# Optimization experiments

Hardware: AMD Instinct MI355X
Metric: run time of the kernel (lower is better)

The kernel has to match this reference:

```python
import jax, jax.numpy as jnp
import numpy as np

C_CURV = 1.0  # hyperbolic curvature (init kwarg c)
EPS = 1e-7


def _to_ball(v, max_norm=0.8):
    # rescale rows to lie strictly inside the unit Poincare ball
    n = jnp.linalg.norm(v, axis=-1, keepdims=True)
    return v * (max_norm / (n + 1.0))


def setup_inputs() -> dict:
    key = jax.random.key(0)
    k1, k2 = jax.random.split(key)
    B, C, D = 32768, 2048, 512
    z_mix = _to_ball(jax.random.normal(k1, (B, D), dtype=jnp.float32))
    prototypes = _to_ball(jax.random.normal(k2, (C, D), dtype=jnp.float32))
    repel_margin = jnp.float32(2.0)
    return {"z_mix": z_mix, "prototypes": prototypes, "repel_margin": repel_margin}


def dist_matrix(x, y, c):
    # Poincare-ball pairwise distance (arccosh form):
    # d(x,y) = arccosh(1 + 2c||x-y||^2 / ((1-c||x||^2)(1-c||y||^2))) / sqrt(c)
    x2 = jnp.sum(x * x, axis=-1)            # (B,)
    y2 = jnp.sum(y * y, axis=-1)            # (C,)
    xy = jnp.einsum('bd,cd->bc', x, y)      # (B, C)
    sqdist = jnp.maximum(x2[:, None] + y2[None, :] - 2.0 * xy, 0.0)
    denom = (1.0 - c * x2)[:, None] * (1.0 - c * y2)[None, :]
    arg = 1.0 + 2.0 * c * sqdist / jnp.maximum(denom, EPS)
    return jnp.arccosh(jnp.maximum(arg, 1.0 + EPS)) / jnp.sqrt(c)


def reference(z_mix, prototypes, repel_margin):
    dist2proto = dist_matrix(z_mix, prototypes, C_CURV)   # (B, C)
    min_dist = jnp.min(dist2proto, axis=1)                # (B,)
    return jnp.mean(jax.nn.relu(repel_margin - min_dist))
```

## Files before the change

kernel.cpp:

```cpp
#include <hip/hip_runtime.h>
#include <stdint.h>

#define EPS_F 1e-7f

typedef float f32x4 __attribute__((ext_vector_type(4)));

union A8 { uint2 u2; long l; };

__device__ __forceinline__ unsigned cvt4(float a, float b, float c, float d) {
  int v = __builtin_amdgcn_cvt_pk_fp8_f32(a, b, 0, false);
  return (unsigned)__builtin_amdgcn_cvt_pk_fp8_f32(c, d, v, true);
}

__global__ __launch_bounds__(256) void prep_kernel(
    const float* __restrict__ protos, uint8_t* __restrict__ wsB,
    float* __restrict__ y2a, float* __restrict__ rya,
    float* __restrict__ out) {
  const int lane = threadIdx.x & 63;
  const int w    = threadIdx.x >> 6;
  const int kp2  = lane >> 2, q = lane & 3;
  const int sl0  = 8 * kp2 + q;
  const int sl1  = sl0 + 4;
#pragma unroll
  for (int i = 0; i < 4; ++i) {
    int c = (blockIdx.x * 4 + w) * 4 + i;
    const float4* p = (const float4*)(protos + (size_t)c * 512 + lane * 8);
    float4 f0 = p[0], f1 = p[1];
    float s = f0.x*f0.x + f0.y*f0.y + f0.z*f0.z + f0.w*f0.w
            + f1.x*f1.x + f1.y*f1.y + f1.z*f1.z + f1.w*f1.w;
#pragma unroll
    for (int off = 32; off > 0; off >>= 1) s += __shfl_xor(s, off, 64);
    if (lane == 0) { y2a[c] = s; rya[c] = 1.f / (1.f - s); }
    unsigned ux = cvt4(f0.x, f0.y, f0.z, f0.w);
    unsigned uy = cvt4(f1.x, f1.y, f1.z, f1.w);
    uint4 ch;
    ch.x = __shfl((int)ux, sl0, 64);
    ch.y = __shfl((int)uy, sl0, 64);
    ch.z = __shfl((int)ux, sl1, 64);
    ch.w = __shfl((int)uy, sl1, 64);
    if (lane < 32) {
      int g = c >> 4, cl = c & 15;
      ((uint4*)wsB)[((size_t)g * 8 + kp2) * 64 + q * 16 + cl] = ch;
    }
  }
  if (blockIdx.x == 0 && threadIdx.x == 0) out[0] = 0.f;
}

__global__ __launch_bounds__(256, 2) void gemm_min_kernel(
    const float* __restrict__ z, const uint8_t* __restrict__ wsB,
    const float* __restrict__ y2a, const float* __restrict__ rya,
    const float* __restrict__ marg, float* __restrict__ out) {
  __shared__ uint8_t As[32 * 1024];
  __shared__ float x2s[64];
  __shared__ float rxs[64];
  __shared__ float minbuf[64][4];

  const int tid  = threadIdx.x;
  const int lane = tid & 63;
  const int w    = tid >> 6;
  const int q    = lane >> 4;
  const int l15  = lane & 15;
  const size_t rowbase = (size_t)blockIdx.x * 64;

  {
    const float* rp0 = z + (rowbase + w * 16 + l15) * 512;
    float s = 0.f;
#pragma unroll
    for (int j = 0; j < 8; ++j) {
      const float* rp = rp0 + j * 64 + q * 8;
      float4 a0 = ((const float4*)rp)[0];
      float4 a1 = ((const float4*)rp)[1];
      float4 b0 = ((const float4*)(rp + 32))[0];
      float4 b1 = ((const float4*)(rp + 32))[1];
      s += a0.x*a0.x + a0.y*a0.y + a0.z*a0.z + a0.w*a0.w
         + a1.x*a1.x + a1.y*a1.y + a1.z*a1.z + a1.w*a1.w
         + b0.x*b0.x + b0.y*b0.y + b0.z*b0.z + b0.w*b0.w
         + b1.x*b1.x + b1.y*b1.y + b1.z*b1.z + b1.w*b1.w;
      uint4 ch;
      ch.x = cvt4(a0.x, a0.y, a0.z, a0.w);
      ch.y = cvt4(a1.x, a1.y, a1.z, a1.w);
      ch.z = cvt4(b0.x, b0.y, b0.z, b0.w);
      ch.w = cvt4(b1.x, b1.y, b1.z, b1.w);
      ((uint4*)As)[(j * 4 + w) * 64 + lane] = ch;
    }
    s += __shfl_xor(s, 16, 64);
    s += __shfl_xor(s, 32, 64);
    if (lane < 16) { x2s[w * 16 + lane] = s; rxs[w * 16 + lane] = 1.f / (1.f - s); }
  }
  __syncthreads();

  float x2r[4][4];
#pragma unroll
  for (int rf = 0; rf < 4; ++rf) {
    float4 x4 = *(const float4*)&x2s[rf * 16 + q * 4];
    x2r[rf][0] = x4.x; x2r[rf][1] = x4.y; x2r[rf][2] = x4.z; x2r[rf][3] = x4.w;
  }

  const uint4* Ap = (const uint4*)As;
  const uint4* Bg = (const uint4*)wsB;

  uint4 B0w[4], B1w[4];
#pragma unroll
  for (int i = 0; i < 4; ++i) {
    B0w[i] = Bg[(size_t)(w * 256 + i) * 64 + lane];
    B1w[i] = Bg[(size_t)(w * 256 + 8 + i) * 64 + lane];
  }

  float tmin[4][4];
#pragma unroll
  for (int rf = 0; rf < 4; ++rf)
#pragma unroll
    for (int r = 0; r < 4; ++r) tmin[rf][r] = 3.4e38f;

  const float* y2p = y2a + w * 512 + l15;
  const float* ryp = rya + w * 512 + l15;

#pragma clang loop unroll(disable)
  for (int s = 0; s < 16; ++s) {
    f32x4 acc[4][2];
#pragma unroll
    for (int rf = 0; rf < 4; ++rf) {
      f32x4 z4 = {0.f, 0.f, 0.f, 0.f};
      acc[rf][0] = z4; acc[rf][1] = z4;
    }
    float y2v0 = y2p[s * 32],      ryv0 = ryp[s * 32];
    float y2v1 = y2p[s * 32 + 16], ryv1 = ryp[s * 32 + 16];

#pragma unroll
    for (int kp2 = 0; kp2 < 8; ++kp2) {
      uint4 bu0 = B0w[kp2 & 3];
      uint4 bu1 = B1w[kp2 & 3];
      {
        int ip = s * 8 + kp2 + 4;
        int sp = ip >> 3, kq = ip & 7;
        size_t c0 = (size_t)(w * 256 + sp * 16 + kq) * 64 + lane;
        B0w[kp2 & 3] = Bg[c0];
        B1w[kp2 & 3] = Bg[c0 + 8 * 64];
      }
      A8 b0lo, b0hi, b1lo, b1hi;
      b0lo.u2 = make_uint2(bu0.x, bu0.y); b0hi.u2 = make_uint2(bu0.z, bu0.w);
      b1lo.u2 = make_uint2(bu1.x, bu1.y); b1hi.u2 = make_uint2(bu1.z, bu1.w);
#pragma unroll
      for (int rf = 0; rf < 4; ++rf) {
        uint4 av = Ap[(kp2 * 4 + rf) * 64 + lane];
        A8 alo, ahi;
        alo.u2 = make_uint2(av.x, av.y);
        ahi.u2 = make_uint2(av.z, av.w);
        acc[rf][0] = __builtin_amdgcn_mfma_f32_16x16x32_fp8_fp8(
            alo.l, b0lo.l, acc[rf][0], 0, 0, 0);
        acc[rf][1] = __builtin_amdgcn_mfma_f32_16x16x32_fp8_fp8(
            alo.l, b1lo.l, acc[rf][1], 0, 0, 0);
        acc[rf][0] = __builtin_amdgcn_mfma_f32_16x16x32_fp8_fp8(
            ahi.l, b0hi.l, acc[rf][0], 0, 0, 0);
        acc[rf][1] = __builtin_amdgcn_mfma_f32_16x16x32_fp8_fp8(
            ahi.l, b1hi.l, acc[rf][1], 0, 0, 0);
      }
    }

#pragma unroll
    for (int rf = 0; rf < 4; ++rf) {
#pragma unroll
      for (int r = 0; r < 4; ++r) {
        float xv = x2r[rf][r];
        float u0 = fmaxf(fmaf(-2.f, acc[rf][0][r], xv + y2v0), 0.f) * ryv0;
        float u1 = fmaxf(fmaf(-2.f, acc[rf][1][r], xv + y2v1), 0.f) * ryv1;
        tmin[rf][r] = fminf(tmin[rf][r], fminf(u0, u1));
      }
    }
  }

#pragma unroll
  for (int rf = 0; rf < 4; ++rf) {
#pragma unroll
    for (int r = 0; r < 4; ++r) {
      float v = tmin[rf][r];
      v = fminf(v, __shfl_xor(v, 1, 64));
      v = fminf(v, __shfl_xor(v, 2, 64));
      v = fminf(v, __shfl_xor(v, 4, 64));
      v = fminf(v, __shfl_xor(v, 8, 64));
      if (l15 == 0) minbuf[rf * 16 + q * 4 + r][w] = v;
    }
  }
  __syncthreads();

  if (w == 0) {
    float m = fminf(fminf(minbuf[lane][0], minbuf[lane][1]),
                    fminf(minbuf[lane][2], minbuf[lane][3]));
    float t = m * rxs[lane];
    float arg = fmaxf(fmaf(2.f, t, 1.f), 1.f + EPS_F);
    float contrib = fmaxf(marg[0] - acoshf(arg), 0.f);
#pragma unroll
    for (int off = 32; off > 0; off >>= 1) contrib += __shfl_xor(contrib, off, 64);
    if (lane == 0) atomicAdd(out, contrib * (1.0f / 32768.f));
  }
}

extern "C" void kernel_launch(void* const* d_in, const int* in_sizes, int n_in,
                              void* d_out, int out_size, void* d_ws, size_t ws_size,
                              hipStream_t stream) {
  const float* z      = (const float*)d_in[0];
  const float* protos = (const float*)d_in[1];
  const float* marg   = (const float*)d_in[2];
  float* out = (float*)d_out;
  uint8_t* wsB = (uint8_t*)d_ws;
  float* y2a = (float*)((char*)d_ws + (1 << 20) + 192 * 1024);
  float* rya = y2a + 2048;

  prep_kernel<<<128, 256, 0, stream>>>(protos, wsB, y2a, rya, out);
  gemm_min_kernel<<<512, 256, 0, stream>>>(z, wsB, y2a, rya, marg, out);
}
```

Baseline: 154.5 us.

## Split prototype dimension across two blocks per row slab with atomicMin merge

Each 64-row slab is now handled by two blocks, one per half of the prototypes, doubling the grid to 1024 blocks. The per-row minimum is merged through an atomicMin on float bits in a workspace, and a new final kernel applies acosh, the margin relu and the mean. Launch bounds are raised to 4 blocks per CU and the x2 values are reloaded from shared memory instead of held in registers, which lowers register pressure. The cost is that each half re-reads and re-converts the z slab to fp8, plus a third kernel launch and extra global atomics.

```diff
diff --git a/kernel.cpp b/kernel.cpp
--- a/kernel.cpp
+++ b/kernel.cpp
@@ -15,7 +15,7 @@
 __global__ __launch_bounds__(256) void prep_kernel(
     const float* __restrict__ protos, uint8_t* __restrict__ wsB,
     float* __restrict__ y2a, float* __restrict__ rya,
-    float* __restrict__ out) {
+    unsigned* __restrict__ minws, float* __restrict__ out) {
   const int lane = threadIdx.x & 63;
   const int w    = threadIdx.x >> 6;
   const int kp2  = lane >> 2, q = lane & 3;
@@ -43,16 +43,16 @@
       ((uint4*)wsB)[((size_t)g * 8 + kp2) * 64 + q * 16 + cl] = ch;
     }
   }
+  minws[blockIdx.x * 256 + threadIdx.x] = 0x7F800000u;
   if (blockIdx.x == 0 && threadIdx.x == 0) out[0] = 0.f;
 }
 
-__global__ __launch_bounds__(256, 2) void gemm_min_kernel(
+__global__ __launch_bounds__(256, 4) void gemm_min_kernel(
     const float* __restrict__ z, const uint8_t* __restrict__ wsB,
     const float* __restrict__ y2a, const float* __restrict__ rya,
-    const float* __restrict__ marg, float* __restrict__ out) {
+    unsigned* __restrict__ minws, float* __restrict__ x2ws) {
   __shared__ uint8_t As[32 * 1024];
   __shared__ float x2s[64];
-  __shared__ float rxs[64];
   __shared__ float minbuf[64][4];
 
   const int tid  = threadIdx.x;
@@ -60,7 +60,9 @@
   const int w    = tid >> 6;
   const int q    = lane >> 4;
   const int l15  = lane & 15;
-  const size_t rowbase = (size_t)blockIdx.x * 64;
+  const int half = blockIdx.x >> 9;
+  const int slab = blockIdx.x & 511;
+  const size_t rowbase = (size_t)slab * 64;
 
   {
     const float* rp0 = z + (rowbase + w * 16 + l15) * 512;
@@ -85,25 +87,21 @@
     }
     s += __shfl_xor(s, 16, 64);
     s += __shfl_xor(s, 32, 64);
-    if (lane < 16) { x2s[w * 16 + lane] = s; rxs[w * 16 + lane] = 1.f / (1.f - s); }
+    if (lane < 16) {
+      x2s[w * 16 + lane] = s;
+      if (half == 0) x2ws[rowbase + w * 16 + lane] = s;
+    }
   }
   __syncthreads();
 
-  float x2r[4][4];
-#pragma unroll
-  for (int rf = 0; rf < 4; ++rf) {
-    float4 x4 = *(const float4*)&x2s[rf * 16 + q * 4];
-    x2r[rf][0] = x4.x; x2r[rf][1] = x4.y; x2r[rf][2] = x4.z; x2r[rf][3] = x4.w;
-  }
-
   const uint4* Ap = (const uint4*)As;
-  const uint4* Bg = (const uint4*)wsB;
+  const uint4* Bgw = (const uint4*)wsB + ((size_t)(half * 512 + w * 128)) * 64 + lane;
 
   uint4 B0w[4], B1w[4];
 #pragma unroll
   for (int i = 0; i < 4; ++i) {
-    B0w[i] = Bg[(size_t)(w * 256 + i) * 64 + lane];
-    B1w[i] = Bg[(size_t)(w * 256 + 8 + i) * 64 + lane];
+    B0w[i] = Bgw[(size_t)i * 64];
+    B1w[i] = Bgw[(size_t)(i + 8) * 64];
   }
 
   float tmin[4][4];
@@ -112,11 +110,11 @@
 #pragma unroll
     for (int r = 0; r < 4; ++r) tmin[rf][r] = 3.4e38f;
 
-  const float* y2p = y2a + w * 512 + l15;
-  const float* ryp = rya + w * 512 + l15;
+  const float* y2p = y2a + half * 1024 + w * 256 + l15;
+  const float* ryp = rya + half * 1024 + w * 256 + l15;
 
 #pragma clang loop unroll(disable)
-  for (int s = 0; s < 16; ++s) {
+  for (int s = 0; s < 8; ++s) {
     f32x4 acc[4][2];
 #pragma unroll
     for (int rf = 0; rf < 4; ++rf) {
@@ -133,9 +131,9 @@
       {
         int ip = s * 8 + kp2 + 4;
         int sp = ip >> 3, kq = ip & 7;
-        size_t c0 = (size_t)(w * 256 + sp * 16 + kq) * 64 + lane;
-        B0w[kp2 & 3] = Bg[c0];
-        B1w[kp2 & 3] = Bg[c0 + 8 * 64];
+        size_t c0 = (size_t)(sp * 16 + kq) * 64;
+        B0w[kp2 & 3] = Bgw[c0];
+        B1w[kp2 & 3] = Bgw[c0 + 8 * 64];
       }
       A8 b0lo, b0hi, b1lo, b1hi;
       b0lo.u2 = make_uint2(bu0.x, bu0.y); b0hi.u2 = make_uint2(bu0.z, bu0.w);
@@ -159,9 +157,10 @@
 
 #pragma unroll
     for (int rf = 0; rf < 4; ++rf) {
+      float4 x4 = *(const float4*)&x2s[rf * 16 + q * 4];
 #pragma unroll
       for (int r = 0; r < 4; ++r) {
-        float xv = x2r[rf][r];
+        float xv = (r == 0) ? x4.x : (r == 1) ? x4.y : (r == 2) ? x4.z : x4.w;
         float u0 = fmaxf(fmaf(-2.f, acc[rf][0][r], xv + y2v0), 0.f) * ryv0;
         float u1 = fmaxf(fmaf(-2.f, acc[rf][1][r], xv + y2v1), 0.f) * ryv1;
         tmin[rf][r] = fminf(tmin[rf][r], fminf(u0, u1));
@@ -186,13 +185,27 @@
   if (w == 0) {
     float m = fminf(fminf(minbuf[lane][0], minbuf[lane][1]),
                     fminf(minbuf[lane][2], minbuf[lane][3]));
-    float t = m * rxs[lane];
-    float arg = fmaxf(fmaf(2.f, t, 1.f), 1.f + EPS_F);
-    float contrib = fmaxf(marg[0] - acoshf(arg), 0.f);
-#pragma unroll
-    for (int off = 32; off > 0; off >>= 1) contrib += __shfl_xor(contrib, off, 64);
-    if (lane == 0) atomicAdd(out, contrib * (1.0f / 32768.f));
-  }
+    atomicMin(&minws[rowbase + lane], __float_as_uint(m));
+  }
+}
+
+__global__ __launch_bounds__(256) void final_kernel(
+    const unsigned* __restrict__ minws, const float* __restrict__ x2ws,
+    const float* __restrict__ marg, float* __restrict__ out) {
+  __shared__ float red[4];
+  int idx  = blockIdx.x * 256 + threadIdx.x;
+  int lane = threadIdx.x & 63;
+  int w    = threadIdx.x >> 6;
+  float u  = __uint_as_float(minws[idx]);
+  float t  = u / (1.f - x2ws[idx]);
+  float arg = fmaxf(fmaf(2.f, t, 1.f), 1.f + EPS_F);
+  float c   = fmaxf(marg[0] - acoshf(arg), 0.f);
+#pragma unroll
+  for (int off = 32; off > 0; off >>= 1) c += __shfl_xor(c, off, 64);
+  if (lane == 0) red[w] = c;
+  __syncthreads();
+  if (threadIdx.x == 0)
+    atomicAdd(out, (red[0] + red[1] + red[2] + red[3]) * (1.0f / 32768.f));
 }
 
 extern "C" void kernel_launch(void* const* d_in, const int* in_sizes, int n_in,
@@ -203,9 +216,13 @@
   const float* marg   = (const float*)d_in[2];
   float* out = (float*)d_out;
   uint8_t* wsB = (uint8_t*)d_ws;
-  float* y2a = (float*)((char*)d_ws + (1 << 20) + 192 * 1024);
-  float* rya = y2a + 2048;
-
-  prep_kernel<<<128, 256, 0, stream>>>(protos, wsB, y2a, rya, out);
-  gemm_min_kernel<<<512, 256, 0, stream>>>(z, wsB, y2a, rya, marg, out);
-}
+  char* p = (char*)d_ws + (1 << 20) + 192 * 1024;
+  float*    y2a   = (float*)p;            p += 8 * 1024;
+  float*    rya   = (float*)p;            p += 8 * 1024;
+  unsigned* minws = (unsigned*)p;         p += 128 * 1024;
+  float*    x2ws  = (float*)p;
+
+  prep_kernel<<<128, 256, 0, stream>>>(protos, wsB, y2a, rya, minws, out);
+  gemm_min_kernel<<<1024, 256, 0, stream>>>(z, wsB, y2a, rya, minws, x2ws);
+  final_kernel<<<128, 256, 0, stream>>>(minws, x2ws, marg, out);
+}
```

Result: slower. 334.0 us (+116.2%).

## Double wavefronts per block, splitting prototype columns across eight waves

Applied to the files above, without the earlier changes.

The block grows from 256 to 512 threads (8 waves). Each wave now covers 256 prototypes instead of 512, and the A-tile conversion and row-norm computation are split across two wave groups by K half. This is meant to add latency hiding and occupancy, since more waves share the same 32 KB LDS A tile. In exchange it needs 8-way min merging, and register pressure under launch_bounds(512,2) may force spills.

```diff
diff --git a/kernel.cpp b/kernel.cpp
--- a/kernel.cpp
+++ b/kernel.cpp
@@ -46,27 +46,28 @@
   if (blockIdx.x == 0 && threadIdx.x == 0) out[0] = 0.f;
 }
 
-__global__ __launch_bounds__(256, 2) void gemm_min_kernel(
+__global__ __launch_bounds__(512, 2) void gemm_min_kernel(
     const float* __restrict__ z, const uint8_t* __restrict__ wsB,
     const float* __restrict__ y2a, const float* __restrict__ rya,
     const float* __restrict__ marg, float* __restrict__ out) {
   __shared__ uint8_t As[32 * 1024];
-  __shared__ float x2s[64];
-  __shared__ float rxs[64];
-  __shared__ float minbuf[64][4];
+  __shared__ float x2p[2][64];
+  __shared__ float minbuf[64][8];
 
   const int tid  = threadIdx.x;
   const int lane = tid & 63;
   const int w    = tid >> 6;
+  const int wk   = w >> 2;
+  const int wr   = w & 3;
   const int q    = lane >> 4;
   const int l15  = lane & 15;
   const size_t rowbase = (size_t)blockIdx.x * 64;
 
   {
-    const float* rp0 = z + (rowbase + w * 16 + l15) * 512;
+    const float* rp0 = z + (rowbase + wr * 16 + l15) * 512 + wk * 256;
     float s = 0.f;
 #pragma unroll
-    for (int j = 0; j < 8; ++j) {
+    for (int j = 0; j < 4; ++j) {
       const float* rp = rp0 + j * 64 + q * 8;
       float4 a0 = ((const float4*)rp)[0];
       float4 a1 = ((const float4*)rp)[1];
@@ -81,29 +82,31 @@
       ch.y = cvt4(a1.x, a1.y, a1.z, a1.w);
       ch.z = cvt4(b0.x, b0.y, b0.z, b0.w);
       ch.w = cvt4(b1.x, b1.y, b1.z, b1.w);
-      ((uint4*)As)[(j * 4 + w) * 64 + lane] = ch;
+      ((uint4*)As)[((wk * 4 + j) * 4 + wr) * 64 + lane] = ch;
     }
     s += __shfl_xor(s, 16, 64);
     s += __shfl_xor(s, 32, 64);
-    if (lane < 16) { x2s[w * 16 + lane] = s; rxs[w * 16 + lane] = 1.f / (1.f - s); }
+    if (lane < 16) x2p[wk][wr * 16 + lane] = s;
   }
   __syncthreads();
 
   float x2r[4][4];
 #pragma unroll
   for (int rf = 0; rf < 4; ++rf) {
-    float4 x4 = *(const float4*)&x2s[rf * 16 + q * 4];
-    x2r[rf][0] = x4.x; x2r[rf][1] = x4.y; x2r[rf][2] = x4.z; x2r[rf][3] = x4.w;
+    float4 xa = *(const float4*)&x2p[0][rf * 16 + q * 4];
+    float4 xb = *(const float4*)&x2p[1][rf * 16 + q * 4];
+    x2r[rf][0] = xa.x + xb.x; x2r[rf][1] = xa.y + xb.y;
+    x2r[rf][2] = xa.z + xb.z; x2r[rf][3] = xa.w + xb.w;
   }
 
   const uint4* Ap = (const uint4*)As;
-  const uint4* Bg = (const uint4*)wsB;
+  const uint4* Bgw = (const uint4*)wsB + (size_t)(w * 128) * 64 + lane;
 
   uint4 B0w[4], B1w[4];
 #pragma unroll
   for (int i = 0; i < 4; ++i) {
-    B0w[i] = Bg[(size_t)(w * 256 + i) * 64 + lane];
-    B1w[i] = Bg[(size_t)(w * 256 + 8 + i) * 64 + lane];
+    B0w[i] = Bgw[(size_t)i * 64];
+    B1w[i] = Bgw[(size_t)(i + 8) * 64];
   }
 
   float tmin[4][4];
@@ -112,11 +115,11 @@
 #pragma unroll
     for (int r = 0; r < 4; ++r) tmin[rf][r] = 3.4e38f;
 
-  const float* y2p = y2a + w * 512 + l15;
-  const float* ryp = rya + w * 512 + l15;
+  const float* y2p = y2a + w * 256 + l15;
+  const float* ryp = rya + w * 256 + l15;
 
 #pragma clang loop unroll(disable)
-  for (int s = 0; s < 16; ++s) {
+  for (int s = 0; s < 8; ++s) {
     f32x4 acc[4][2];
 #pragma unroll
     for (int rf = 0; rf < 4; ++rf) {
@@ -133,9 +136,9 @@
       {
         int ip = s * 8 + kp2 + 4;
         int sp = ip >> 3, kq = ip & 7;
-        size_t c0 = (size_t)(w * 256 + sp * 16 + kq) * 64 + lane;
-        B0w[kp2 & 3] = Bg[c0];
-        B1w[kp2 & 3] = Bg[c0 + 8 * 64];
+        size_t c0 = (size_t)(sp * 16 + kq) * 64;
+        B0w[kp2 & 3] = Bgw[c0];
+        B1w[kp2 & 3] = Bgw[c0 + 8 * 64];
       }
       A8 b0lo, b0hi, b1lo, b1hi;
       b0lo.u2 = make_uint2(bu0.x, bu0.y); b0hi.u2 = make_uint2(bu0.z, bu0.w);
@@ -184,9 +187,11 @@
   __syncthreads();
 
   if (w == 0) {
-    float m = fminf(fminf(minbuf[lane][0], minbuf[lane][1]),
-                    fminf(minbuf[lane][2], minbuf[lane][3]));
-    float t = m * rxs[lane];
+    float m = 3.4e38f;
+#pragma unroll
+    for (int j = 0; j < 8; ++j) m = fminf(m, minbuf[lane][j]);
+    float x2 = x2p[0][lane] + x2p[1][lane];
+    float t = m / (1.f - x2);
     float arg = fmaxf(fmaf(2.f, t, 1.f), 1.f + EPS_F);
     float contrib = fmaxf(marg[0] - acoshf(arg), 0.f);
 #pragma unroll
@@ -203,9 +208,10 @@
   const float* marg   = (const float*)d_in[2];
   float* out = (float*)d_out;
   uint8_t* wsB = (uint8_t*)d_ws;
-  float* y2a = (float*)((char*)d_ws + (1 << 20) + 192 * 1024);
-  float* rya = y2a + 2048;
+  char* p = (char*)d_ws + (1 << 20) + 192 * 1024;
+  float* y2a = (float*)p;                 p += 8 * 1024;
+  float* rya = (float*)p;
 
   prep_kernel<<<128, 256, 0, stream>>>(protos, wsB, y2a, rya, out);
-  gemm_min_kernel<<<512, 256, 0, stream>>>(z, wsB, y2a, rya, marg, out);
-}
+  gemm_min_kernel<<<512, 512, 0, stream>>>(z, wsB, y2a, rya, marg, out);
+}
```

Measured after the change: 168.8 us. 1.09x slower.
